# Performance work log

Measured on AMD Instinct MI355X. Metric: run time of the kernel, lower is better.

Reference implementation:

```python
import jax, jax.numpy as jnp
import numpy as np

BATCH = 256
SEED = 0


def build_tree(seed=SEED):
    """Synthetic 3-level hierarchy, BFS node numbering (children of level d are
    exactly the contiguous block of level d+1 nodes). Returns (num_nodes, levels)
    where levels[d] = (parents, flat_inputs_index, concat_children, P, M)."""
    rng = np.random.default_rng(seed)
    branch = [(100, 101), (5, 51), (20, 61)]  # (lo, hi) child counts per level
    level_sizes = [1]
    counts = []
    for lo, hi in branch:
        c = rng.integers(lo, hi, size=level_sizes[-1])
        counts.append(c)
        level_sizes.append(int(c.sum()))
    starts = np.concatenate([[0], np.cumsum(level_sizes)])
    num_nodes = int(starts[-1])
    levels = []
    for d in range(3):
        P = level_sizes[d]
        c = counts[d]
        M = int(c.max())
        parents = np.arange(starts[d], starts[d] + P, dtype=np.int32)
        concat_children = np.arange(starts[d + 1], starts[d + 2], dtype=np.int32)
        offs = np.concatenate([[0], np.cumsum(c)[:-1]])
        i = np.repeat(np.arange(P, dtype=np.int64), c)  # row (parent slot)
        j = np.arange(int(c.sum()), dtype=np.int64) - np.repeat(offs, c)  # col within row
        flat_idx = (i * M + j).astype(np.int32)
        levels.append((parents, flat_idx, concat_children, P, M))
    return num_nodes, levels


def setup_inputs() -> dict:
    num_nodes, levels = build_tree()
    key = jax.random.key(0)
    scores = jax.random.normal(key, (BATCH, num_nodes), dtype=jnp.float32)
    out = {"scores": scores}
    for d, (p, f, c, P, M) in enumerate(levels):
        out[f"p{d}"] = jnp.asarray(p)
        out[f"f{d}"] = jnp.asarray(f)
        out[f"c{d}"] = jnp.asarray(c)
        out[f"P{d}"] = P
        out[f"M{d}"] = M
    return out


def _level_reduce(out, parents, flat_idx, concat_children, P, M):
    # Gather ragged children scores into a padded [B, P, M] buffer (-inf pad),
    # logsumexp over children, then max-combine into the parent entries.
    B = out.shape[0]
    flat = jnp.full((B, P * M), -jnp.inf, dtype=out.dtype)
    flat = flat.at[:, flat_idx].set(out[:, concat_children])
    lse = jax.nn.logsumexp(flat.reshape(B, P, M), axis=-1)  # [B, P]
    return out.at[:, parents].set(jnp.maximum(out[:, parents], lse))


def reference(scores, p0, f0, c0, P0, M0, p1, f1, c1, P1, M1, p2, f2, c2, P2, M2):
    # Bottom-up over levels (deepest first), as in the torch module.
    out = scores
    out = _level_reduce(out, p2, f2, c2, P2, M2)
    out = _level_reduce(out, p1, f1, c1, P1, M1)
    out = _level_reduce(out, p0, f0, c0, P0, M0)
    return out
```

## Files before the change

kernel.cpp:

```cpp
#include <hip/hip_runtime.h>

static constexpr int B = 256;

__global__ void build_offs3(
    const int* __restrict__ f0, int n0, const int* __restrict__ M0p, int P0, int* __restrict__ offs0,
    const int* __restrict__ f1, int n1, const int* __restrict__ M1p, int P1, int* __restrict__ offs1,
    const int* __restrict__ f2, int n2, const int* __restrict__ M2p, int P2, int* __restrict__ offs2)
{
    int k = blockIdx.x * blockDim.x + threadIdx.x;
    if (k < n0) {
        int M = M0p[0];
        int v = f0[k];
        int i = v / M;
        if (v - i * M == 0) offs0[i] = k;
    }
    if (k < n1) {
        int M = M1p[0];
        int v = f1[k];
        int i = v / M;
        if (v - i * M == 0) offs1[i] = k;
    }
    if (k < n2) {
        int M = M2p[0];
        int v = f2[k];
        int i = v / M;
        if (v - i * M == 0) offs2[i] = k;
    }
    if (k == 0) { offs0[P0] = n0; offs1[P1] = n1; offs2[P2] = n2; }
}

template <bool COPY>
__global__ void __launch_bounds__(256) level_reduce_chunk(
    const float* __restrict__ scores, float* __restrict__ out,
    const int* __restrict__ offs,
    const int* __restrict__ pbase_p,
    const int* __restrict__ cbase_p,
    int P, int num_nodes)
{
    constexpr int PPB = 64;
    constexpr int MAXSPAN = PPB * 60;
    __shared__ float vals[MAXSPAN];

    const int tid  = threadIdx.x;
    const int p0   = blockIdx.x * PPB;
    const int pcnt = min(PPB, P - p0);
    const int b    = blockIdx.y;

    const int cbase = cbase_p[0];
    const int pbase = pbase_p[0];
    const int e0 = offs[p0];
    const int e1 = offs[p0 + pcnt];
    const int span = e1 - e0;

    const size_t row = (size_t)b * num_nodes;
    const float* __restrict__ src  = (COPY ? scores : out) + row + cbase + e0;
    float*       __restrict__ dstc = out + row + cbase + e0;

    for (int k = tid; k < span; k += 256) {
        float v = src[k];
        if (COPY) dstc[k] = v;
        vals[k] = v;
    }
    __syncthreads();

    const int p = tid >> 2;
    const int q = tid & 3;
    if (p < pcnt) {
        const int sa  = offs[p0 + p];
        const int cnt = offs[p0 + p + 1] - sa;
        const int s   = sa - e0;
        const float NEG = -3.0e38f;
        float m = NEG;
        for (int k = q; k < cnt; k += 4) m = fmaxf(m, vals[s + k]);
        m = fmaxf(m, __shfl_xor(m, 1));
        m = fmaxf(m, __shfl_xor(m, 2));
        float e = 0.0f;
        for (int k = q; k < cnt; k += 4) e += __expf(vals[s + k] - m);
        e += __shfl_xor(e, 1);
        e += __shfl_xor(e, 2);
        if (q == 0) {
            const int pnode = pbase + p0 + p;
            float lse = m + __logf(e);
            out[row + pnode] = fmaxf(scores[row + pnode], lse);
        }
    }
}

extern "C" void kernel_launch(void* const* d_in, const int* in_sizes, int n_in,
                              void* d_out, int out_size, void* d_ws, size_t ws_size,
                              hipStream_t stream) {
    const float* scores = (const float*)d_in[0];
    const int* p0 = (const int*)d_in[1];
    const int* f0 = (const int*)d_in[2];
    const int* M0 = (const int*)d_in[5];
    const int* p1 = (const int*)d_in[6];
    const int* f1 = (const int*)d_in[7];
    const int* M1 = (const int*)d_in[10];
    const int* p2 = (const int*)d_in[11];
    const int* f2 = (const int*)d_in[12];
    const int* M2 = (const int*)d_in[15];
    const int* c0 = (const int*)d_in[3];
    const int* c1 = (const int*)d_in[8];
    const int* c2 = (const int*)d_in[13];
    float* out = (float*)d_out;

    const int n0 = in_sizes[2];
    const int n1 = in_sizes[7];
    const int n2 = in_sizes[12];
    const int P0v = in_sizes[1];
    const int P1v = in_sizes[6];
    const int P2v = in_sizes[11];
    const int num_nodes = out_size / B;

    int* offs0 = (int*)d_ws;
    int* offs1 = offs0 + (P0v + 2);
    int* offs2 = offs1 + (P1v + 2);

    int nmax = n2 > n1 ? n2 : n1;
    if (n0 > nmax) nmax = n0;
    build_offs3<<<(nmax + 255) / 256, 256, 0, stream>>>(
        f0, n0, M0, P0v, offs0,
        f1, n1, M1, P1v, offs1,
        f2, n2, M2, P2v, offs2);

    constexpr int PPB = 64;
    dim3 g2((P2v + PPB - 1) / PPB, B);
    dim3 g1((P1v + PPB - 1) / PPB, B);
    dim3 g0((P0v + PPB - 1) / PPB, B);
    level_reduce_chunk<true ><<<g2, 256, 0, stream>>>(scores, out, offs2, p2, c2, P2v, num_nodes);
    level_reduce_chunk<false><<<g1, 256, 0, stream>>>(scores, out, offs1, p1, c1, P1v, num_nodes);
    level_reduce_chunk<false><<<g0, 256, 0, stream>>>(scores, out, offs0, p0, c0, P0v, num_nodes);
}
```

Baseline: 266.3 us.

## Fuse upper two tree levels into one kernel and vectorize leaf copy

The level-1 and level-0 reductions are merged into a single per-batch-row kernel. It stages all level-1 children in LDS, computes level-1 logsumexp, and then reduces the 100 root children in shared memory, which removes one launch and a global round trip. The leaf kernel now copies scores with aligned float4 loads and stores, plus scalar prologue and epilogue. Its per-parent inner loop is fully unrolled to 15 elements with clamped, masked loads. The fused kernel hardcodes limits (5128 staged values, 128 level-1 parents, level-0 children ≤128), and the leaf loop assumes at most 60 children per parent.

```diff
diff --git a/kernel.cpp b/kernel.cpp
--- a/kernel.cpp
+++ b/kernel.cpp
@@ -29,17 +29,15 @@
     if (k == 0) { offs0[P0] = n0; offs1[P1] = n1; offs2[P2] = n2; }
 }
 
-template <bool COPY>
-__global__ void __launch_bounds__(256) level_reduce_chunk(
+__global__ void __launch_bounds__(256) leaf_reduce(
     const float* __restrict__ scores, float* __restrict__ out,
     const int* __restrict__ offs,
-    const int* __restrict__ pbase_p,
-    const int* __restrict__ cbase_p,
+    const int* __restrict__ pbase_p, const int* __restrict__ cbase_p,
     int P, int num_nodes)
 {
     constexpr int PPB = 64;
     constexpr int MAXSPAN = PPB * 60;
-    __shared__ float vals[MAXSPAN];
+    __shared__ __align__(16) float vals[MAXSPAN + 8];
 
     const int tid  = threadIdx.x;
     const int p0   = blockIdx.x * PPB;
@@ -53,13 +51,28 @@
     const int span = e1 - e0;
 
     const size_t row = (size_t)b * num_nodes;
-    const float* __restrict__ src  = (COPY ? scores : out) + row + cbase + e0;
-    float*       __restrict__ dstc = out + row + cbase + e0;
-
-    for (int k = tid; k < span; k += 256) {
-        float v = src[k];
-        if (COPY) dstc[k] = v;
-        vals[k] = v;
+    const size_t g0  = row + cbase + e0;
+    const float* __restrict__ src = scores + g0;
+    float*       __restrict__ dst = out + g0;
+
+    const int a   = (int)((4 - (g0 & 3)) & 3);
+    const int pro = a < span ? a : span;
+    const int pad = (4 - a) & 3;
+
+    if (tid < pro) { float v = src[tid]; dst[tid] = v; vals[pad + tid] = v; }
+    const int nq = (span - pro) >> 2;
+    const float4* __restrict__ src4 = (const float4*)(src + pro);
+    float4*       __restrict__ dst4 = (float4*)(dst + pro);
+    float4*                    lds4 = (float4*)(vals + pad + pro);
+    for (int j = tid; j < nq; j += 256) {
+        float4 v = src4[j];
+        dst4[j] = v;
+        lds4[j] = v;
+    }
+    const int rem = span - pro - (nq << 2);
+    if (tid < rem) {
+        int k = pro + (nq << 2) + tid;
+        float v = src[k]; dst[k] = v; vals[pad + k] = v;
     }
     __syncthreads();
 
@@ -68,20 +81,102 @@
     if (p < pcnt) {
         const int sa  = offs[p0 + p];
         const int cnt = offs[p0 + p + 1] - sa;
-        const int s   = sa - e0;
+        const int s   = sa - e0 + pad;
+        const int hi  = span + pad - 1;
         const float NEG = -3.0e38f;
+        float x[15];
+#pragma unroll
+        for (int k = 0; k < 15; ++k) {
+            int idx = s + q + 4 * k;
+            idx = idx < hi ? idx : hi;
+            float v = vals[idx];
+            x[k] = (q + 4 * k < cnt) ? v : NEG;
+        }
         float m = NEG;
-        for (int k = q; k < cnt; k += 4) m = fmaxf(m, vals[s + k]);
+#pragma unroll
+        for (int k = 0; k < 15; ++k) m = fmaxf(m, x[k]);
         m = fmaxf(m, __shfl_xor(m, 1));
         m = fmaxf(m, __shfl_xor(m, 2));
         float e = 0.0f;
-        for (int k = q; k < cnt; k += 4) e += __expf(vals[s + k] - m);
+#pragma unroll
+        for (int k = 0; k < 15; ++k) e += __expf(x[k] - m);
         e += __shfl_xor(e, 1);
         e += __shfl_xor(e, 2);
         if (q == 0) {
             const int pnode = pbase + p0 + p;
             float lse = m + __logf(e);
             out[row + pnode] = fmaxf(scores[row + pnode], lse);
+        }
+    }
+}
+
+__global__ void __launch_bounds__(256) upper_reduce(
+    const float* __restrict__ scores, float* __restrict__ out,
+    const int* __restrict__ offs1,
+    const int* __restrict__ p1base_p, const int* __restrict__ c1base_p,
+    const int* __restrict__ p0base_p,
+    int P1, int n1, int n0, int num_nodes)
+{
+    __shared__ __align__(16) float vals[5128];
+    __shared__ float upd[128];
+
+    const int tid = threadIdx.x;
+    const int b   = blockIdx.x;
+    const size_t row = (size_t)b * num_nodes;
+
+    const int c1base = c1base_p[0];
+    const int p1base = p1base_p[0];
+    const int p0base = p0base_p[0];
+
+    const size_t g0 = row + c1base;
+    const float* __restrict__ src = out + g0;
+    const int a   = (int)((4 - (g0 & 3)) & 3);
+    const int pro = a < n1 ? a : n1;
+    const int pad = (4 - a) & 3;
+    if (tid < pro) vals[pad + tid] = src[tid];
+    const int nq = (n1 - pro) >> 2;
+    const float4* __restrict__ src4 = (const float4*)(src + pro);
+    float4*                    lds4 = (float4*)(vals + pad + pro);
+    for (int j = tid; j < nq; j += 256) lds4[j] = src4[j];
+    const int rem = n1 - pro - (nq << 2);
+    if (tid < rem) { int k = pro + (nq << 2) + tid; vals[pad + k] = src[k]; }
+    __syncthreads();
+
+    const int p = tid >> 1;
+    const int q = tid & 1;
+    const float NEG = -3.0e38f;
+    if (p < P1) {
+        const int sa  = offs1[p];
+        const int cnt = offs1[p + 1] - sa;
+        const int s   = sa + pad;
+        float m = NEG;
+        for (int k = q; k < cnt; k += 2) m = fmaxf(m, vals[s + k]);
+        m = fmaxf(m, __shfl_xor(m, 1));
+        float e = 0.0f;
+        for (int k = q; k < cnt; k += 2) e += __expf(vals[s + k] - m);
+        e += __shfl_xor(e, 1);
+        if (q == 0) {
+            const int pnode = p1base + p;
+            float lse = m + __logf(e);
+            float v = fmaxf(scores[row + pnode], lse);
+            out[row + pnode] = v;
+            upd[p] = v;
+        }
+    }
+    __syncthreads();
+
+    if (tid < 64) {
+        float x0 = (tid      < n0) ? upd[tid]      : NEG;
+        float x1 = (tid + 64 < n0) ? upd[tid + 64] : NEG;
+        float m = fmaxf(x0, x1);
+#pragma unroll
+        for (int off = 32; off; off >>= 1) m = fmaxf(m, __shfl_xor(m, off));
+        float e = __expf(x0 - m) + __expf(x1 - m);
+#pragma unroll
+        for (int off = 32; off; off >>= 1) e += __shfl_xor(e, off);
+        if (tid == 0) {
+            float lse = m + __logf(e);
+            out[row + p0base] = fmaxf(scores[row + p0base], lse);
         }
     }
 }
@@ -99,7 +194,6 @@
     const int* p2 = (const int*)d_in[11];
     const int* f2 = (const int*)d_in[12];
     const int* M2 = (const int*)d_in[15];
-    const int* c0 = (const int*)d_in[3];
     const int* c1 = (const int*)d_in[8];
     const int* c2 = (const int*)d_in[13];
     float* out = (float*)d_out;
@@ -125,9 +219,7 @@
 
     constexpr int PPB = 64;
     dim3 g2((P2v + PPB - 1) / PPB, B);
-    dim3 g1((P1v + PPB - 1) / PPB, B);
-    dim3 g0((P0v + PPB - 1) / PPB, B);
-    level_reduce_chunk<true ><<<g2, 256, 0, stream>>>(scores, out, offs2, p2, c2, P2v, num_nodes);
-    level_reduce_chunk<false><<<g1, 256, 0, stream>>>(scores, out, offs1, p1, c1, P1v, num_nodes);
-    level_reduce_chunk<false><<<g0, 256, 0, stream>>>(scores, out, offs0, p0, c0, P0v, num_nodes);
-}
+    leaf_reduce<<<g2, 256, 0, stream>>>(scores, out, offs2, p2, c2, P2v, num_nodes);
+    upper_reduce<<<dim3(B), 256, 0, stream>>>(scores, out, offs1, p1, c1, p0,
+                                              P1v, n1, n0, num_nodes);
+}
```

New measurement: 257.9 us. 3.2% less time.
